# Kernel optimization log

Hardware: AMD Instinct MI355X
Metric: run time of the kernel (lower is better)

The kernel has to match this reference:

```python
import jax, jax.numpy as jnp
import numpy as np

INV_SQRT2 = np.float32(1.0 / np.sqrt(2.0))


def _vortex_adj():
    # Vortex-math doubling map on digital roots 1..9: v -> 2v mod 9 (9 if 0),
    # plus self-loops; row-normalized message-passing matrix over 9 nodes.
    A = np.zeros((9, 9), np.float32)
    for i in range(9):
        t = (2 * (i + 1)) % 9
        t = 9 if t == 0 else t
        A[t - 1, i] = 1.0
        A[i, i] = 1.0
    A = A / A.sum(axis=1, keepdims=True)
    return jnp.asarray(A)


def setup_inputs() -> dict:
    key = jax.random.key(0)
    ks = jax.random.split(key, 24)
    B, D, H, O = 16384, 512, 512, 128
    Hq, Hw = H // 4, H // 2
    g = lambda k, shp, fan: jax.random.normal(k, shp, jnp.float32) * np.float32(fan ** -0.5)
    return {
        "x": jax.random.normal(ks[0], (B, D), jnp.float32),
        "W_in": g(ks[1], (D, 9 * H), D), "b_in": jnp.zeros((9 * H,), jnp.float32),
        "W_dr": g(ks[2], (H, H), H), "b_dr": jnp.zeros((H,), jnp.float32),
        "W_hyp": g(ks[3], (H, H), H), "b_hyp": jnp.zeros((H,), jnp.float32),
        "Wq_r": g(ks[4], (Hq, Hq), H), "Wq_i": g(ks[5], (Hq, Hq), H),
        "Wq_j": g(ks[6], (Hq, Hq), H), "Wq_k": g(ks[7], (Hq, Hq), H),
        "b_quat": jnp.zeros((H,), jnp.float32),
        "W_low": g(ks[8], (Hw, Hw), Hw), "W_high": g(ks[9], (Hw, Hw), Hw),
        "b_wav": jnp.zeros((H,), jnp.float32),
        "attn_Wq": g(ks[10], (3, H, H), H), "attn_Wk": g(ks[11], (3, H, H), H),
        "attn_Wv": g(ks[12], (3, H, H), H), "attn_Wo": g(ks[13], (3, H, H), H),
        "gamma": jnp.ones((3, H), jnp.float32), "beta": jnp.zeros((3, H), jnp.float32),
        "W_out": g(ks[14], (H, O), H), "b_out": jnp.zeros((O,), jnp.float32),
    }


def _attention(z, Wq, Wk, Wv, Wo, h):
    # single-head attention over the 9 vortex nodes
    q, k, v = z @ Wq, z @ Wk, z @ Wv
    a = jax.nn.softmax(jnp.einsum('bqh,bkh->bqk', q, k) / jnp.sqrt(jnp.float32(h)), axis=-1)
    return jnp.einsum('bqk,bkh->bqh', a, v) @ Wo


def _drnorm(z, g, b):
    mu = jnp.mean(z, axis=-1, keepdims=True)
    var = jnp.mean((z - mu) ** 2, axis=-1, keepdims=True)
    return g * (z - mu) * jax.lax.rsqrt(var + np.float32(1e-5)) + b


def reference(x, W_in, b_in, W_dr, b_dr, W_hyp, b_hyp, Wq_r, Wq_i, Wq_j, Wq_k,
              b_quat, W_low, W_high, b_wav, attn_Wq, attn_Wk, attn_Wv, attn_Wo,
              gamma, beta, W_out, b_out):
    B = x.shape[0]
    H = W_dr.shape[0]
    adj = _vortex_adj()
    agg = lambda z: jnp.einsum('mn,bnh->bmh', adj, z)

    # input_processor + DigitalRootUnit: [B,D] -> [B,9,H]
    p = jax.nn.leaky_relu(x @ W_in + b_in, 0.01)
    nf = jnp.tanh(p.reshape(B, 9, H) @ W_dr + b_dr)

    # ---- layer 0: HyperbolicVortexLayer ----
    m = agg(nf)
    v = jnp.tanh(m @ W_hyp + b_hyp)
    a = _attention(v, attn_Wq[0], attn_Wk[0], attn_Wv[0], attn_Wo[0], H)
    nf = v + _drnorm(a, gamma[0], beta[0])

    # ---- layer 1: QuaternionVortexLayer (Hamilton-product linear) ----
    m = agg(nf)
    q4 = m.reshape(B, 9, 4, H // 4)
    r, i, j, k = q4[:, :, 0], q4[:, :, 1], q4[:, :, 2], q4[:, :, 3]
    r2 = r @ Wq_r - i @ Wq_i - j @ Wq_j - k @ Wq_k
    i2 = r @ Wq_i + i @ Wq_r + j @ Wq_k - k @ Wq_j
    j2 = r @ Wq_j - i @ Wq_k + j @ Wq_r + k @ Wq_i
    k2 = r @ Wq_k + i @ Wq_j - j @ Wq_i + k @ Wq_r
    v = jnp.tanh(jnp.concatenate([r2, i2, j2, k2], axis=-1) + b_quat)
    a = _attention(v, attn_Wq[1], attn_Wk[1], attn_Wv[1], attn_Wo[1], H)
    nf = v + _drnorm(a, gamma[1], beta[1])

    # ---- layer 2: WaveletVortexLayer (Haar analysis/synthesis) ----
    m = agg(nf)
    xe, xo = m[..., 0::2], m[..., 1::2]
    low = (xe + xo) * INV_SQRT2
    high = (xe - xo) * INV_SQRT2
    low2, high2 = low @ W_low, high @ W_high
    even = (low2 + high2) * INV_SQRT2
    odd = (low2 - high2) * INV_SQRT2
    rec = jnp.stack([even, odd], axis=-1).reshape(B, 9, H)
    v = jnp.tanh(rec + b_wav)
    a = _attention(v, attn_Wq[2], attn_Wk[2], attn_Wv[2], attn_Wo[2], H)
    nf = v + _drnorm(a, gamma[2], beta[2])

    # readout from node 9 (index 8)
    return nf[:, 8, :] @ W_out + b_out
```

## Files before the change

### kernel.cpp

```cpp
#include <hip/hip_runtime.h>

typedef unsigned short u16;
typedef unsigned int u32;
typedef float f32x4 __attribute__((ext_vector_type(4)));
typedef __bf16 bf16x8 __attribute__((ext_vector_type(8)));
typedef u16 u16x8 __attribute__((ext_vector_type(8)));

__device__ __forceinline__ float bf2f(u16 v) {
  union { u32 u; float f; } c; c.u = ((u32)v) << 16; return c.f;
}
__device__ __forceinline__ u16 f2bf(float f) {
  union { float f; u32 u; } c; c.f = f;
  c.u += 0x7fffu + ((c.u >> 16) & 1u);
  return (u16)(c.u >> 16);
}
__device__ __forceinline__ float fast_tanh(float x) {
  float e = __expf(2.0f * x);
  return 1.0f - 2.0f / (e + 1.0f);
}
__device__ __forceinline__ void gload16(const void* g, void* l) {
  __builtin_amdgcn_global_load_lds((const __attribute__((address_space(1))) void*)g,
                                   (__attribute__((address_space(3))) void*)l, 16, 0, 0);
}
__device__ __forceinline__ bf16x8 ldfrag(const u16* p) {
  return __builtin_bit_cast(bf16x8, *(const u16x8*)p);
}
__device__ __forceinline__ int xcd_swizzle() {
  const int nwg = (int)gridDim.x, orig = (int)blockIdx.x;
  const int q = nwg >> 3, r = nwg & 7;
  const int xcd = orig & 7, idx = orig >> 3;
  return (xcd < r ? xcd * (q + 1) : r * (q + 1) + (xcd - r) * q) + idx;
}

__global__ __launch_bounds__(256) void conv_bf(const float* __restrict__ s,
                                               u16* __restrict__ d, long n) {
  const long i = (long)blockIdx.x * 256 + threadIdx.x;
  if (i < n) d[i] = f2bf(s[i]);
}

__global__ __launch_bounds__(256) void trans_conv(const float* __restrict__ src,
                                                  u16* __restrict__ dst,
                                                  int K, int N, int batch) {
  const long total = (long)batch * K * N;
  const long idx = (long)blockIdx.x * 256 + threadIdx.x;
  if (idx >= total) return;
  const long l = idx / ((long)K * N);
  const long rem = idx - l * (long)K * N;
  const int n = (int)(rem / K);
  const int k = (int)(rem - (long)n * K);
  dst[idx] = f2bf(src[l * (long)K * N + (long)k * N + n]);
}

__global__ __launch_bounds__(256) void transf32(const float* __restrict__ src,
                                                float* __restrict__ dst) {
  const long idx = (long)blockIdx.x * 256 + threadIdx.x;
  const long l = idx >> 18;
  const int rem = (int)(idx & 262143);
  const int n = rem >> 9, a = rem & 511;
  dst[idx] = src[l * 262144 + (long)a * 512 + n];
}

__global__ __launch_bounds__(256) void build_quat(const float* __restrict__ wr,
                                                  const float* __restrict__ wi,
                                                  const float* __restrict__ wj,
                                                  const float* __restrict__ wk,
                                                  u16* __restrict__ dst) {
  const int idx = blockIdx.x * 256 + threadIdx.x;
  const int n = idx >> 9, k = idx & 511;
  const int kb = k >> 7, kc = k & 127, nb = n >> 7, nc = n & 127;
  const float* const srcs[4] = {wr, wi, wj, wk};
  const float sgn[4][4] = {{1,1,1,1},{-1,1,-1,1},{-1,1,1,-1},{-1,-1,1,1}};
  dst[idx] = f2bf(sgn[kb][nb] * srcs[kb ^ nb][kc * 128 + nc]);
}

__global__ __launch_bounds__(256) void build_wav(const float* __restrict__ lo,
                                                 const float* __restrict__ hi,
                                                 u16* __restrict__ dst) {
  const int idx = blockIdx.x * 256 + threadIdx.x;
  const int n = idx >> 9, k = idx & 511;
  const int d = k >> 1, c = n >> 1;
  const float a = lo[d * 256 + c], b = hi[d * 256 + c];
  dst[idx] = f2bf(((k ^ n) & 1) ? 0.5f * (a - b) : 0.5f * (a + b));
}

__global__ __launch_bounds__(256) void fold_nt(const float* __restrict__ Wq,
                                               const float* __restrict__ Wk,
                                               const float* __restrict__ Wv,
                                               const float* __restrict__ WoT,
                                               u16* __restrict__ dst) {
  const int bx = blockIdx.x;
  const int slot = bx >> 6, l = slot >> 1, isvo = slot & 1;
  const float* L = isvo ? WoT + (size_t)l * 262144 : Wk + (size_t)l * 262144;
  const float* R = isvo ? Wv + (size_t)l * 262144 : Wq + (size_t)l * 262144;
  u16* D = dst + (size_t)l * 524288 + (size_t)isvo * 262144;
  const int t = bx & 63;
  const int n0 = (t >> 3) << 6, k0 = (t & 7) << 6;
  __shared__ float Lt[64][65];
  __shared__ float Rt[64][65];
  const int tid = threadIdx.x;
  const int tr = tid >> 4, tc = tid & 15;
  float acc[4][4] = {};
  for (int a0 = 0; a0 < 512; a0 += 64) {
    __syncthreads();
    #pragma unroll
    for (int r = 0; r < 4; ++r) {
      const int idx = r * 256 + tid;
      const int row = idx >> 4, c4 = (idx & 15) << 2;
      const f32x4 lv = *(const f32x4*)&L[(size_t)(n0 + row) * 512 + a0 + c4];
      const f32x4 rv = *(const f32x4*)&R[(size_t)(k0 + row) * 512 + a0 + c4];
      #pragma unroll
      for (int u = 0; u < 4; ++u) { Lt[row][c4 + u] = lv[u]; Rt[row][c4 + u] = rv[u]; }
    }
    __syncthreads();
    #pragma unroll 4
    for (int kk = 0; kk < 64; ++kk) {
      float lv[4], rv[4];
      #pragma unroll
      for (int i = 0; i < 4; ++i) lv[i] = Lt[tr * 4 + i][kk];
      #pragma unroll
      for (int j = 0; j < 4; ++j) rv[j] = Rt[tc * 4 + j][kk];
      #pragma unroll
      for (int i = 0; i < 4; ++i)
        #pragma unroll
        for (int j = 0; j < 4; ++j) acc[i][j] += lv[i] * rv[j];
    }
  }
  #pragma unroll
  for (int i = 0; i < 4; ++i)
    #pragma unroll
    for (int j = 0; j < 4; ++j)
      D[(size_t)(n0 + tr * 4 + i) * 512 + k0 + tc * 4 + j] = f2bf(acc[i][j]);
}

template<int EPI>
__global__ __launch_bounds__(256, 3)
void gemm_k(const u16* __restrict__ A, int arow, const u16* __restrict__ BT,
            u16* __restrict__ C, float* __restrict__ Cf,
            const float* __restrict__ bias, int N, int K) {
  __shared__ u16 lsA[128 * 64];
  __shared__ u16 lsB[128 * 64];
  const int tid = threadIdx.x;
  const int nblk = N >> 7;
  const int bx = xcd_swizzle();
  const int bm = bx / nblk;
  const int bn = bx % nblk;
  const long m0 = (long)bm << 7;
  const int n0 = bn << 7;
  const int w = tid >> 6, lane = tid & 63;
  const int wrow = ((w >> 1) & 1) << 6;
  const int wcol = (w & 1) << 6;
  const int lr = lane & 15, lg = lane >> 4;

  f32x4 acc[4][4];
  #pragma unroll
  for (int i = 0; i < 4; ++i)
    #pragma unroll
    for (int j = 0; j < 4; ++j) acc[i][j] = (f32x4){0.f, 0.f, 0.f, 0.f};

  for (int kt = 0; kt < K; kt += 64) {
    __syncthreads();
    #pragma unroll
    for (int r = 0; r < 4; ++r) {
      const int chunk = r * 256 + tid;
      const int row = chunk >> 3, cc = (chunk & 7) << 3;
      gload16(A + (m0 + row) * (long)arow + kt + cc, &lsA[chunk * 8]);
    }
    #pragma unroll
    for (int r = 0; r < 4; ++r) {
      const int chunk = r * 256 + tid;
      const int row = chunk >> 3, cc = (chunk & 7) << 3;
      gload16(BT + (size_t)(n0 + row) * K + kt + cc, &lsB[chunk * 8]);
    }
    __syncthreads();
    #pragma unroll
    for (int kk = 0; kk < 64; kk += 32) {
      bf16x8 af[4], bfr[4];
      #pragma unroll
      for (int m = 0; m < 4; ++m)
        af[m] = ldfrag(&lsA[(wrow + m * 16 + lr) * 64 + kk + lg * 8]);
      #pragma unroll
      for (int n = 0; n < 4; ++n)
        bfr[n] = ldfrag(&lsB[(wcol + n * 16 + lr) * 64 + kk + lg * 8]);
      #pragma unroll
      for (int m = 0; m < 4; ++m)
        #pragma unroll
        for (int n = 0; n < 4; ++n)
          acc[m][n] = __builtin_amdgcn_mfma_f32_16x16x32_bf16(
              af[m], bfr[n], acc[m][n], 0, 0, 0);
    }
  }
  #pragma unroll
  for (int m = 0; m < 4; ++m) {
    const long rbase = m0 + wrow + m * 16 + lg * 4;
    #pragma unroll
    for (int n = 0; n < 4; ++n) {
      const int col = n0 + wcol + n * 16 + lr;
      float bv = 0.f;
      if (EPI == 1 || EPI == 2 || EPI == 3) bv = bias[col];
      #pragma unroll
      for (int j = 0; j < 4; ++j) {
        float v = acc[m][n][j];
        const long row = rbase + j;
        if (EPI == 1) { v += bv; v = v > 0.f ? v : 0.01f * v; }
        if (EPI == 2) { v += bv; v = fast_tanh(v); }
        if (EPI == 3) { v += bv; }
        if (EPI == 3) Cf[row * N + col] = v;
        else          C[row * N + col] = f2bf(v);
      }
    }
  }
}

__global__ __launch_bounds__(256) void agg_k(const u16* __restrict__ z,
                                             u16* __restrict__ mo) {
  const long idx = (long)blockIdx.x * 256 + threadIdx.x;
  const int h0 = (int)(idx & 63) << 3;
  const long row = idx >> 6;
  const long b = row / 9;
  const int node = (int)(row - b * 9);
  const int srcn = (5 * node + 4) % 9;
  const u16x8 a = *(const u16x8*)&z[row * 512 + h0];
  const u16x8 c = *(const u16x8*)&z[(b * 9 + srcn) * 512 + h0];
  u16x8 o;
  #pragma unroll
  for (int u = 0; u < 8; ++u) o[u] = f2bf(0.5f * (bf2f(a[u]) + bf2f(c[u])));
  *(u16x8*)&mo[row * 512 + h0] = o;
}

template<int MODE>
__global__ __launch_bounds__(256, 2)
void attn_fused(const u16* __restrict__ sv, const u16* __restrict__ z,
                const float* __restrict__ gamma, const float* __restrict__ beta,
                u16* __restrict__ outp) {
  __shared__ float laf[4][256];
  const int tid = threadIdx.x;
  const int wv = tid >> 6, lane = tid & 63;
  const long b = (long)blockIdx.x * 4 + wv;
  const long b9 = b * 9;
  const int lr = lane & 15, lg = lane >> 4;
  const int rr = lr > 8 ? 8 : lr;

  f32x4 sacc = {0.f, 0.f, 0.f, 0.f};
  const u16* srow = sv + (b9 + rr) * 1024;
  const u16* zrow = z + (b9 + rr) * 512;
  #pragma unroll
  for (int kc = 0; kc < 16; ++kc) {
    const bf16x8 qa = ldfrag(srow + kc * 32 + lg * 8);
    const bf16x8 kb = ldfrag(zrow + kc * 32 + lg * 8);
    sacc = __builtin_amdgcn_mfma_f32_16x16x32_bf16(qa, kb, sacc, 0, 0, 0);
  }
  const float scale = 0.0441941738241592f;
  #pragma unroll
  for (int r = 0; r < 4; ++r) {
    float s = sacc[r] * scale;
    if (lr > 8) s = -1e30f;
    float mx = s;
    #pragma unroll
    for (int m = 1; m < 16; m <<= 1) mx = fmaxf(mx, __shfl_xor(mx, m, 16));
    const float e = __expf(s - mx);
    float sum = e;
    #pragma unroll
    for (int m = 1; m < 16; m <<= 1) sum += __shfl_xor(sum, m, 16);
    laf[wv][(lg * 4 + r) * 16 + lr] = e / sum;
  }
  __syncthreads();

  constexpr int NR = (MODE == 0) ? 9 : 1;
  float o[NR][8];
  #pragma unroll
  for (int i = 0; i < NR; ++i)
    #pragma unroll
    for (int u = 0; u < 8; ++u) o[i][u] = 0.f;

  #pragma unroll
  for (int j = 0; j < 9; ++j) {
    const u16x8 v8 = *(const u16x8*)&sv[(b9 + j) * 1024 + 512 + lane * 8];
    float vf[8];
    #pragma unroll
    for (int u = 0; u < 8; ++u) vf[u] = bf2f(v8[u]);
    #pragma unroll
    for (int i = 0; i < NR; ++i) {
      const float aij = laf[wv][((MODE == 0) ? i : 8) * 16 + j];
      #pragma unroll
      for (int u = 0; u < 8; ++u) o[i][u] += aij * vf[u];
    }
  }

  const f32x4 g0 = *(const f32x4*)&gamma[lane * 8];
  const f32x4 g1 = *(const f32x4*)&gamma[lane * 8 + 4];
  const f32x4 t0 = *(const f32x4*)&beta[lane * 8];
  const f32x4 t1 = *(const f32x4*)&beta[lane * 8 + 4];
  float gm[8] = {g0[0], g0[1], g0[2], g0[3], g1[0], g1[1], g1[2], g1[3]};
  float bt[8] = {t0[0], t0[1], t0[2], t0[3], t1[0], t1[1], t1[2], t1[3]};

  #pragma unroll
  for (int i = 0; i < NR; ++i) {
    float s1 = 0.f, s2 = 0.f;
    #pragma unroll
    for (int u = 0; u < 8; ++u) { s1 += o[i][u]; s2 += o[i][u] * o[i][u]; }
    #pragma unroll
    for (int m = 1; m < 64; m <<= 1) {
      s1 += __shfl_xor(s1, m, 64); s2 += __shfl_xor(s2, m, 64);
    }
    const float mu = s1 * (1.f / 512.f);
    const float rv = rsqrtf(s2 * (1.f / 512.f) - mu * mu + 1e-5f);
    const int zi = (MODE == 0) ? i : 8;
    const u16x8 z8 = *(const u16x8*)&z[(b9 + zi) * 512 + lane * 8];
    #pragma unroll
    for (int u = 0; u < 8; ++u)
      o[i][u] = bf2f(z8[u]) + gm[u] * (o[i][u] - mu) * rv + bt[u];
  }

  if (MODE == 0) {
    #pragma unroll
    for (int i = 0; i < 9; ++i) {
      const int srcn = (5 * i + 4) % 9;
      u16x8 ov;
      #pragma unroll
      for (int u = 0; u < 8; ++u) ov[u] = f2bf(0.5f * (o[i][u] + o[srcn][u]));
      *(u16x8*)&outp[(b9 + i) * 512 + lane * 8] = ov;
    }
  } else {
    u16x8 ov;
    #pragma unroll
    for (int u = 0; u < 8; ++u) ov[u] = f2bf(o[0][u]);
    *(u16x8*)&outp[b * 512 + lane * 8] = ov;
  }
}

extern "C" void kernel_launch(void* const* d_in, const int* in_sizes, int n_in,
                              void* d_out, int out_size, void* d_ws, size_t ws_size,
                              hipStream_t stream) {
  (void)in_sizes; (void)n_in; (void)out_size;
  const float* x      = (const float*)d_in[0];
  const float* W_in   = (const float*)d_in[1];
  const float* b_in   = (const float*)d_in[2];
  const float* W_dr   = (const float*)d_in[3];
  const float* b_dr   = (const float*)d_in[4];
  const float* W_hyp  = (const float*)d_in[5];
  const float* b_hyp  = (const float*)d_in[6];
  const float* Wq_r   = (const float*)d_in[7];
  const float* Wq_i   = (const float*)d_in[8];
  const float* Wq_j   = (const float*)d_in[9];
  const float* Wq_k   = (const float*)d_in[10];
  const float* b_quat = (const float*)d_in[11];
  const float* W_low  = (const float*)d_in[12];
  const float* W_high = (const float*)d_in[13];
  const float* b_wav  = (const float*)d_in[14];
  const float* aWq    = (const float*)d_in[15];
  const float* aWk    = (const float*)d_in[16];
  const float* aWv    = (const float*)d_in[17];
  const float* aWo    = (const float*)d_in[18];
  const float* gamma  = (const float*)d_in[19];
  const float* beta   = (const float*)d_in[20];
  const float* W_out  = (const float*)d_in[21];
  const float* b_out  = (const float*)d_in[22];
  float* out = (float*)d_out;

  char* ws = (char*)d_ws;
  char* wp = ws;
  u16* WinT   = (u16*)wp;  wp += (size_t)4608 * 512 * 2;
  u16* WdrT   = (u16*)wp;  wp += 524288;
  u16* WhyT   = (u16*)wp;  wp += 524288;
  u16* WquT   = (u16*)wp;  wp += 524288;
  u16* WwvT   = (u16*)wp;  wp += 524288;
  u16* BTqkvo = (u16*)wp;  wp += 3 * 1024 * 512 * 2;
  u16* WouT   = (u16*)wp;  wp += 131072;
  float* WoTf = (float*)wp; wp += 3 * 512 * 512 * 4;
  const size_t woff = (size_t)(wp - ws);

  int nc = 2;
  while (nc < 64 && woff + (size_t)(16384 / nc) * 37888ULL > ws_size) nc *= 2;
  const int CB = 16384 / nc;
  const int CR = CB * 9;

  char* cbase = ws + woff;
  u16* xbf  = (u16*)cbase;
  u16* buf0 = (u16*)(cbase + (size_t)CB * 1024);
  u16* buf1 = buf0 + (size_t)CR * 512;
  u16* sv   = buf1 + (size_t)CR * 512;

  trans_conv<<<9216, 256, 0, stream>>>(W_in, WinT, 512, 4608, 1);
  trans_conv<<<1024, 256, 0, stream>>>(W_dr, WdrT, 512, 512, 1);
  trans_conv<<<1024, 256, 0, stream>>>(W_hyp, WhyT, 512, 512, 1);
  trans_conv<<<256, 256, 0, stream>>>(W_out, WouT, 512, 128, 1);
  build_quat<<<1024, 256, 0, stream>>>(Wq_r, Wq_i, Wq_j, Wq_k, WquT);
  build_wav<<<1024, 256, 0, stream>>>(W_low, W_high, WwvT);
  transf32<<<3072, 256, 0, stream>>>(aWo, WoTf);
  fold_nt<<<384, 256, 0, stream>>>(aWq, aWk, aWv, WoTf, BTqkvo);

  const int g512 = (CR >> 7) * 4;
  const int g1024 = (CR >> 7) * 8;
  const int rowsDiv4 = CR >> 2;

  for (int c = 0; c < nc; ++c) {
    const size_t b0 = (size_t)c * CB;
    conv_bf<<<CB * 2, 256, 0, stream>>>(x + b0 * 512, xbf, (long)CB * 512);
    gemm_k<1><<<(CB >> 7) * 36, 256, 0, stream>>>(
        xbf, 512, WinT, buf0, nullptr, b_in, 4608, 512);
    gemm_k<2><<<g512, 256, 0, stream>>>(
        buf0, 512, WdrT, buf1, nullptr, b_dr, 512, 512);
    agg_k<<<rowsDiv4, 256, 0, stream>>>(buf1, sv);
    gemm_k<2><<<g512, 256, 0, stream>>>(
        sv, 512, WhyT, buf0, nullptr, b_hyp, 512, 512);

    for (int l = 0; l < 3; ++l) {
      gemm_k<0><<<g1024, 256, 0, stream>>>(
          buf0, 512, BTqkvo + (size_t)l * 524288, sv, nullptr, nullptr,
          1024, 512);
      if (l < 2) {
        attn_fused<0><<<CB / 4, 256, 0, stream>>>(
            sv, buf0, gamma + l * 512, beta + l * 512, buf1);
        gemm_k<2><<<g512, 256, 0, stream>>>(
            buf1, 512, (l == 0) ? WquT : WwvT, buf0, nullptr,
            (l == 0) ? b_quat : b_wav, 512, 512);
      } else {
        attn_fused<2><<<CB / 4, 256, 0, stream>>>(
            sv, buf0, gamma + 2 * 512, beta + 2 * 512, xbf);
      }
    }
    gemm_k<3><<<CB >> 7, 256, 0, stream>>>(
        xbf, 512, WouT, nullptr, out + b0 * 128, b_out, 128, 512);
  }
}
```

Measured before the change: 1.942 ms.

## Add 256x256-tile 8-wave bf16 MFMA GEMM with double-buffered LDS for main GEMMs

Introduces a new GEMM kernel using 256x256 output tiles with 512 threads (8 waves, 128x64 per wave) and double-buffered LDS prefetch via global_load_lds, with explicit barriers and s_setprio around MFMA bursts. All large GEMMs (input projection, DR, hyperbolic, QKVO, quaternion/wavelet) switch to it, with grid sizes adjusted. The larger tiles raise arithmetic intensity and cut global/LDS traffic per FLOP, at the cost of more registers (256 accumulators), 128KB LDS per block, and fewer blocks per grid, which can hurt occupancy and tail balance. The old gemm_k launch bounds also change to 2 blocks per CU.

```diff
diff --git a/kernel.cpp b/kernel.cpp
--- a/kernel.cpp
+++ b/kernel.cpp
@@ -24,6 +24,11 @@
 }
 __device__ __forceinline__ bf16x8 ldfrag(const u16* p) {
   return __builtin_bit_cast(bf16x8, *(const u16x8*)p);
+}
+__device__ __forceinline__ void BAR() {
+  asm volatile("" ::: "memory");
+  __builtin_amdgcn_s_barrier();
+  asm volatile("" ::: "memory");
 }
 __device__ __forceinline__ int xcd_swizzle() {
   const int nwg = (int)gridDim.x, orig = (int)blockIdx.x;
@@ -133,7 +138,116 @@
 }
 
 template<int EPI>
-__global__ __launch_bounds__(256, 3)
+__global__ __launch_bounds__(512, 2)
+void gemm256(const u16* __restrict__ A, const u16* __restrict__ BT,
+             u16* __restrict__ C, const float* __restrict__ bias,
+             int N, int K) {
+  __shared__ u16 L[65536];
+  const int tid = threadIdx.x;
+  const int nblk = N >> 8;
+  const int bx = xcd_swizzle();
+  const int bm = bx / nblk, bn = bx % nblk;
+  const long m0 = (long)bm << 8;
+  const int n0 = bn << 8;
+  const int wid = tid >> 6, lane = tid & 63;
+  const int wr = wid >> 2, wc = wid & 3;
+  const int lr = lane & 15, lg = lane >> 4;
+  const int innerU16 = lr * 32 + ((lg * 8) ^ ((lr & 8) ? 16 : 0));
+
+  int srow[4], scol[4], sdst[4];
+  #pragma unroll
+  for (int j = 0; j < 4; ++j) {
+    const int c = tid + 512 * j;
+    const int s = c >> 6, w = c & 63, lrow = w >> 2;
+    const int lcol = ((w & 3) * 8) ^ ((lrow & 8) ? 16 : 0);
+    srow[j] = (s >> 1) * 16 + lrow;
+    scol[j] = (s & 1) * 32 + lcol;
+    sdst[j] = c * 8;
+  }
+
+  f32x4 acc[8][4];
+  #pragma unroll
+  for (int i = 0; i < 8; ++i)
+    #pragma unroll
+    for (int j = 0; j < 4; ++j) acc[i][j] = (f32x4){0.f, 0.f, 0.f, 0.f};
+
+  const int NT = K >> 6;
+  #pragma unroll
+  for (int j = 0; j < 4; ++j)
+    gload16(A + (m0 + srow[j]) * (long)K + scol[j], &L[sdst[j]]);
+  #pragma unroll
+  for (int j = 0; j < 4; ++j)
+    gload16(BT + (size_t)(n0 + srow[j]) * K + scol[j], &L[16384 + sdst[j]]);
+
+  #pragma unroll 1
+  for (int t = 0; t < NT; ++t) {
+    const int par = t & 1;
+    if (t + 1 < NT) {
+      const int kt = (t + 1) << 6;
+      const int pb = (par ^ 1) << 15;
+      #pragma unroll
+      for (int j = 0; j < 4; ++j)
+        gload16(A + (m0 + srow[j]) * (long)K + kt + scol[j], &L[pb + sdst[j]]);
+      #pragma unroll
+      for (int j = 0; j < 4; ++j)
+        gload16(BT + (size_t)(n0 + srow[j]) * K + kt + scol[j],
+                &L[pb + 16384 + sdst[j]]);
+      asm volatile("s_waitcnt vmcnt(8)" ::: "memory");
+    } else {
+      asm volatile("s_waitcnt vmcnt(0)" ::: "memory");
+    }
+    BAR();
+    const u16* LA = &L[par << 15];
+    const u16* LB = LA + 16384;
+    #pragma unroll
+    for (int p = 0; p < 4; ++p) {
+      const int mq = (p >> 1) * 4, nq = (p & 1) * 2;
+      bf16x8 af[2][4], bf[2][2];
+      #pragma unroll
+      for (int kkb = 0; kkb < 2; ++kkb) {
+        #pragma unroll
+        for (int i = 0; i < 4; ++i)
+          af[kkb][i] = ldfrag(&LA[((wr * 8 + mq + i) * 2 + kkb) * 512 + innerU16]);
+        #pragma unroll
+        for (int n = 0; n < 2; ++n)
+          bf[kkb][n] = ldfrag(&LB[((wc * 4 + nq + n) * 2 + kkb) * 512 + innerU16]);
+      }
+      BAR();
+      __builtin_amdgcn_s_setprio(1);
+      #pragma unroll
+      for (int kkb = 0; kkb < 2; ++kkb)
+        #pragma unroll
+        for (int i = 0; i < 4; ++i)
+          #pragma unroll
+          for (int n = 0; n < 2; ++n)
+            acc[mq + i][nq + n] = __builtin_amdgcn_mfma_f32_16x16x32_bf16(
+                af[kkb][i], bf[kkb][n], acc[mq + i][nq + n], 0, 0, 0);
+      __builtin_amdgcn_s_setprio(0);
+      BAR();
+    }
+  }
+
+  #pragma unroll
+  for (int m = 0; m < 8; ++m) {
+    const long rbase = m0 + wr * 128 + m * 16 + lg * 4;
+    #pragma unroll
+    for (int n = 0; n < 4; ++n) {
+      const int col = n0 + wc * 64 + n * 16 + lr;
+      float bv = 0.f;
+      if (EPI == 1 || EPI == 2) bv = bias[col];
+      #pragma unroll
+      for (int j = 0; j < 4; ++j) {
+        float v = acc[m][n][j];
+        if (EPI == 1) { v += bv; v = v > 0.f ? v : 0.01f * v; }
+        if (EPI == 2) { v += bv; v = fast_tanh(v); }
+        C[(rbase + j) * N + col] = f2bf(v);
+      }
+    }
+  }
+}
+
+template<int EPI>
+__global__ __launch_bounds__(256, 2)
 void gemm_k(const u16* __restrict__ A, int arow, const u16* __restrict__ BT,
             u16* __restrict__ C, float* __restrict__ Cf,
             const float* __restrict__ bias, int N, int K) {
@@ -389,30 +503,27 @@
   transf32<<<3072, 256, 0, stream>>>(aWo, WoTf);
   fold_nt<<<384, 256, 0, stream>>>(aWq, aWk, aWv, WoTf, BTqkvo);
 
-  const int g512 = (CR >> 7) * 4;
-  const int g1024 = (CR >> 7) * 8;
+  const int g512 = (CR >> 8) * 2;
+  const int g1024 = (CR >> 8) * 4;
   const int rowsDiv4 = CR >> 2;
 
   for (int c = 0; c < nc; ++c) {
     const size_t b0 = (size_t)c * CB;
     conv_bf<<<CB * 2, 256, 0, stream>>>(x + b0 * 512, xbf, (long)CB * 512);
-    gemm_k<1><<<(CB >> 7) * 36, 256, 0, stream>>>(
-        xbf, 512, WinT, buf0, nullptr, b_in, 4608, 512);
-    gemm_k<2><<<g512, 256, 0, stream>>>(
-        buf0, 512, WdrT, buf1, nullptr, b_dr, 512, 512);
+    gemm256<1><<<(CB >> 8) * 18, 512, 0, stream>>>(
+        xbf, WinT, buf0, b_in, 4608, 512);
+    gemm256<2><<<g512, 512, 0, stream>>>(buf0, WdrT, buf1, b_dr, 512, 512);
     agg_k<<<rowsDiv4, 256, 0, stream>>>(buf1, sv);
-    gemm_k<2><<<g512, 256, 0, stream>>>(
-        sv, 512, WhyT, buf0, nullptr, b_hyp, 512, 512);
+    gemm256<2><<<g512, 512, 0, stream>>>(sv, WhyT, buf0, b_hyp, 512, 512);
 
     for (int l = 0; l < 3; ++l) {
-      gemm_k<0><<<g1024, 256, 0, stream>>>(
-          buf0, 512, BTqkvo + (size_t)l * 524288, sv, nullptr, nullptr,
-          1024, 512);
+      gemm256<0><<<g1024, 512, 0, stream>>>(
+          buf0, BTqkvo + (size_t)l * 524288, sv, nullptr, 1024, 512);
       if (l < 2) {
         attn_fused<0><<<CB / 4, 256, 0, stream>>>(
             sv, buf0, gamma + l * 512, beta + l * 512, buf1);
-        gemm_k<2><<<g512, 256, 0, stream>>>(
-            buf1, 512, (l == 0) ? WquT : WwvT, buf0, nullptr,
+        gemm256<2><<<g512, 512, 0, stream>>>(
+            buf1, (l == 0) ? WquT : WwvT, buf0,
             (l == 0) ? b_quat : b_wav, 512, 512);
       } else {
         attn_fused<2><<<CB / 4, 256, 0, stream>>>(
```

Result: slower. 2.528 ms (+30.2%).
